# Optimization experiments

Measured on AMD Instinct MI355X. Metric: run time of the kernel, lower is better.

Reference implementation:

```python
import jax, jax.numpy as jnp
import numpy as np

N_NODES = 100000
N_EDGES = 1600000
IN_DIM = 256
OUT_DIM = 128


def setup_inputs() -> dict:
    key = jax.random.key(0)
    k1, k2, k3, k4, k5 = jax.random.split(key, 5)
    h = jax.random.normal(k1, (N_NODES, IN_DIM), dtype=jnp.float32)
    # xavier_normal-ish scales for the two weight matrices
    W = jax.random.normal(k2, (IN_DIM, OUT_DIM), dtype=jnp.float32) * (2.0 / np.sqrt(IN_DIM + OUT_DIM))
    a = jax.random.normal(k3, (2 * OUT_DIM,), dtype=jnp.float32) * (2.0 / np.sqrt(2 * OUT_DIM + 1))
    src = jax.random.randint(k4, (N_EDGES,), 0, N_NODES, dtype=jnp.int32)
    dst = jax.random.randint(k5, (N_EDGES,), 0, N_NODES, dtype=jnp.int32)
    return {"h": h, "W": W, "a": a, "src": src, "dst": dst}


def reference(h, W, a, src, dst):
    n = h.shape[0]
    d = W.shape[1]
    z = h @ W  # [N, out_dim]
    # attn_fc([z_src || z_dst]) == z_src @ a[:d] + z_dst @ a[d:]
    el = z @ a[:d]  # [N]
    er = z @ a[d:]  # [N]
    e = jax.nn.leaky_relu(el[src] + er[dst])  # [E], torch default slope 0.01
    # per-destination (segment) softmax, numerically stable
    seg_max = jax.ops.segment_max(e, dst, num_segments=n)
    e_exp = jnp.exp(e - seg_max[dst])
    denom = jax.ops.segment_sum(e_exp, dst, num_segments=n)
    alpha = e_exp / denom[dst]  # [E]
    # weighted scatter-sum of source z into destinations
    h_out = jax.ops.segment_sum(alpha[:, None] * z[src], dst, num_segments=n)
    return h_out
```

## Files before the change

### kernel.cpp

```cpp
#include <hip/hip_runtime.h>
#include <cstdint>
#include <cstddef>

#define N_NODES 100000
#define N_EDGES 1600000
#define IN_DIM  256
#define OUT_DIM 128

#define NBUCK  391
#define BSHIFT 8
#define BNODES 256
#define BCAP   5632
#define EPB    4096

#define ENC_NEG_INF 0x00800000u

typedef __attribute__((ext_vector_type(8))) short bf16x8;
typedef __attribute__((ext_vector_type(4))) float f32x4;

__device__ __forceinline__ unsigned bf16rn(float f) {
    unsigned u = __float_as_uint(f);
    return (u + 0x7FFFu + ((u >> 16) & 1u)) >> 16;
}

__global__ void init_k(int* __restrict__ bucket_cursor)
{
    int i = blockIdx.x * blockDim.x + threadIdx.x;
    if (i < NBUCK) bucket_cursor[i] = 0;
}

__global__ void w16s_k(const float* __restrict__ W, unsigned short* __restrict__ w16s)
{
    int t = blockIdx.x * blockDim.x + threadIdx.x;
    if (t >= IN_DIM * OUT_DIM) return;
    int j  = t & 7;
    int n  = (t >> 3) & 15;
    int q  = (t >> 7) & 3;
    int c  = (t >> 9) & 7;
    int kc = t >> 12;
    int k   = kc * 32 + q * 8 + j;
    int dim = c * 16 + n;
    w16s[t] = (unsigned short)bf16rn(W[k * OUT_DIM + dim]);
}

#define LA_STRIDE 264

__global__ __launch_bounds__(256) void gemm_z_k(
    const float* __restrict__ h, const unsigned short* __restrict__ w16s,
    const float* __restrict__ a,
    unsigned short* __restrict__ z16, float* __restrict__ el, float* __restrict__ er)
{
    __shared__ unsigned short lA[64 * LA_STRIDE];
    const int t  = threadIdx.x;
    const int n0 = blockIdx.x * 64;

    #pragma unroll
    for (int p = 0; p < 16; ++p) {
        int f = p * 256 + t;
        int i = f >> 6;
        int col = (f & 63) * 4;
        float4 v = make_float4(0.f, 0.f, 0.f, 0.f);
        if (n0 + i < N_NODES)
            v = *(const float4*)&h[(size_t)(n0 + i) * IN_DIM + col];
        uint2 pk;
        pk.x = bf16rn(v.x) | (bf16rn(v.y) << 16);
        pk.y = bf16rn(v.z) | (bf16rn(v.w) << 16);
        *(uint2*)&lA[i * LA_STRIDE + col] = pk;
    }
    __syncthreads();

    const int w    = t >> 6;
    const int lane = t & 63;
    const int q    = lane >> 4;
    const int col  = lane & 15;

    f32x4 acc[8];
    #pragma unroll
    for (int c = 0; c < 8; ++c) acc[c] = (f32x4){0.f, 0.f, 0.f, 0.f};

    #pragma unroll
    for (int kc = 0; kc < 8; ++kc) {
        bf16x8 af = *(const bf16x8*)&lA[(w * 16 + col) * LA_STRIDE + kc * 32 + q * 8];
        bf16x8 bfr[8];
        #pragma unroll
        for (int c = 0; c < 8; ++c)
            bfr[c] = *(const bf16x8*)&w16s[((((kc * 8 + c) * 4 + q) * 16) + col) * 8];
        #pragma unroll
        for (int c = 0; c < 8; ++c)
            acc[c] = __builtin_amdgcn_mfma_f32_16x16x32_bf16(af, bfr[c], acc[c], 0, 0, 0);
    }

    float aL[8], aR[8];
    #pragma unroll
    for (int c = 0; c < 8; ++c) {
        aL[c] = a[c * 16 + col];
        aR[c] = a[128 + c * 16 + col];
    }
    #pragma unroll
    for (int r = 0; r < 4; ++r) {
        int node = n0 + w * 16 + q * 4 + r;
        float sl = 0.f, sr = 0.f;
        #pragma unroll
        for (int c = 0; c < 8; ++c) {
            sl += acc[c][r] * aL[c];
            sr += acc[c][r] * aR[c];
        }
        #pragma unroll
        for (int o = 1; o < 16; o <<= 1) {
            sl += __shfl_xor(sl, o, 64);
            sr += __shfl_xor(sr, o, 64);
        }
        if (node < N_NODES) {
            #pragma unroll
            for (int c = 0; c < 8; ++c)
                z16[(size_t)node * OUT_DIM + c * 16 + col] =
                    (unsigned short)bf16rn(acc[c][r]);
            if (col == 0) { el[node] = sl; er[node] = sr; }
        }
    }
}

__global__ __launch_bounds__(256) void partition_k(
    const int* __restrict__ src, const int* __restrict__ dst,
    const float* __restrict__ el, const float* __restrict__ er,
    int* __restrict__ bucket_cursor, unsigned long long* __restrict__ ebuf)
{
    __shared__ int hist[NBUCK];
    __shared__ int gbaseL[NBUCK];
    const int t = threadIdx.x;
    for (int i = t; i < NBUCK; i += 256) hist[i] = 0;
    __syncthreads();

    const int e0 = blockIdx.x * EPB;
    int bucks[16], ranks[16];
    unsigned long long pk[16];
    #pragma unroll
    for (int k = 0; k < 16; ++k) {
        int e = e0 + k * 256 + t;
        bucks[k] = -1;
        if (e < N_EDGES) {
            int s = src[e], d = dst[e];
            float v = el[s] + er[d];
            v = (v > 0.0f) ? v : 0.01f * v;
            int b = d >> BSHIFT;
            bucks[k] = b;
            ranks[k] = atomicAdd(&hist[b], 1);
            pk[k] = ((unsigned long long)__float_as_uint(v) << 32)
                  | ((unsigned)s << BSHIFT) | (unsigned)(d & (BNODES - 1));
        }
    }
    __syncthreads();
    for (int i = t; i < NBUCK; i += 256)
        gbaseL[i] = atomicAdd(&bucket_cursor[i], hist[i]);
    __syncthreads();
    #pragma unroll
    for (int k = 0; k < 16; ++k)
        if (bucks[k] >= 0)
            ebuf[(size_t)bucks[k] * BCAP + gbaseL[bucks[k]] + ranks[k]] = pk[k];
}

__global__ __launch_bounds__(256) void bucket_k(
    const int* __restrict__ bucket_cursor, const unsigned long long* __restrict__ ebuf,
    unsigned long long* __restrict__ perm, int* __restrict__ begA,
    int* __restrict__ endA, float* __restrict__ denomA)
{
    __shared__ int deg[BNODES];
    __shared__ int off[BNODES];
    __shared__ int cur[BNODES];
    __shared__ unsigned emaxL[BNODES];
    __shared__ float denomL[BNODES];
    __shared__ int ssum[256];

    const int b = blockIdx.x;
    const int t = threadIdx.x;
    const int cnt = bucket_cursor[b];
    const unsigned long long* eb = ebuf + (size_t)b * BCAP;
    unsigned long long* pb = perm + (size_t)b * BCAP;

    deg[t] = 0; emaxL[t] = ENC_NEG_INF; denomL[t] = 0.0f;
    __syncthreads();

    for (int i = t; i < cnt; i += 256) {
        unsigned long long pv = eb[i];
        int ld = (int)(pv & (BNODES - 1));
        unsigned e32 = (unsigned)(pv >> 32);
        unsigned enc = (e32 & 0x80000000u) ? ~e32 : (e32 | 0x80000000u);
        atomicAdd(&deg[ld], 1);
        atomicMax(&emaxL[ld], enc);
    }
    __syncthreads();

    int d  = deg[t];
    int pd = (d + 3) & ~3;
    ssum[t] = pd;
    __syncthreads();
    for (int o = 1; o < 256; o <<= 1) {
        int v = (t >= o) ? ssum[t - o] : 0;
        __syncthreads();
        ssum[t] += v;
        __syncthreads();
    }
    int excl = ssum[t] - pd;
    off[t] = excl; cur[t] = excl;
    __syncthreads();

    for (int i = t; i < cnt; i += 256) {
        unsigned long long pv = eb[i];
        int ld = (int)(pv & (BNODES - 1));
        unsigned s = (unsigned)((pv >> BSHIFT) & 0x1FFFFu);
        float e = __uint_as_float((unsigned)(pv >> 32));
        unsigned u = emaxL[ld];
        float mx = (u & 0x80000000u) ? __uint_as_float(u ^ 0x80000000u)
                                     : __uint_as_float(~u);
        float w = __expf(e - mx);
        atomicAdd(&denomL[ld], w);
        int p = atomicAdd(&cur[ld], 1);
        pb[p] = ((unsigned long long)__float_as_uint(w) << 32) | s;
    }
    __syncthreads();

    int n = b * BNODES + t;
    if (n < N_NODES) {
        int o  = off[t];
        int gb = b * BCAP + o;
        begA[n]   = gb;
        endA[n]   = gb + pd;
        denomA[n] = denomL[t];
        for (int j = o + d; j < o + pd; ++j) pb[j] = 0ull;
    }
}

__global__ __launch_bounds__(256) void node_pass_k(
    const int* __restrict__ begA, const int* __restrict__ endA,
    const float* __restrict__ denomA, const unsigned long long* __restrict__ perm,
    const unsigned* __restrict__ z16, float* __restrict__ out)
{
    int n    = (blockIdx.x * blockDim.x + threadIdx.x) >> 6;
    int lane = threadIdx.x & 63;
    if (n >= N_NODES) return;
    int beg = begA[n], end = endA[n];

    float acc0 = 0.0f, acc1 = 0.0f;
    if (end > beg) {
        const uint4* pp = (const uint4*)perm;
        #pragma unroll 2
        for (int i = (beg >> 2); i < (end >> 2); ++i) {
            uint4 pA = pp[2 * i];
            uint4 pB = pp[2 * i + 1];
            unsigned q0 = z16[(size_t)pA.x * 64 + lane];
            unsigned q1 = z16[(size_t)pA.z * 64 + lane];
            unsigned q2 = z16[(size_t)pB.x * 64 + lane];
            unsigned q3 = z16[(size_t)pB.z * 64 + lane];
            float w0 = __uint_as_float(pA.y);
            float w1 = __uint_as_float(pA.w);
            float w2 = __uint_as_float(pB.y);
            float w3 = __uint_as_float(pB.w);
            acc0 += w0 * __uint_as_float(q0 << 16)
                  + w1 * __uint_as_float(q1 << 16)
                  + w2 * __uint_as_float(q2 << 16)
                  + w3 * __uint_as_float(q3 << 16);
            acc1 += w0 * __uint_as_float(q0 & 0xFFFF0000u)
                  + w1 * __uint_as_float(q1 & 0xFFFF0000u)
                  + w2 * __uint_as_float(q2 & 0xFFFF0000u)
                  + w3 * __uint_as_float(q3 & 0xFFFF0000u);
        }
        float inv = 1.0f / denomA[n];
        acc0 *= inv; acc1 *= inv;
    }
    *(float2*)&out[(size_t)n * OUT_DIM + lane * 2] = make_float2(acc0, acc1);
}

extern "C" void kernel_launch(void* const* d_in, const int* in_sizes, int n_in,
                              void* d_out, int out_size, void* d_ws, size_t ws_size,
                              hipStream_t stream)
{
    (void)in_sizes; (void)n_in; (void)out_size; (void)ws_size;
    const float* h = (const float*)d_in[0];
    const float* W = (const float*)d_in[1];
    const float* a = (const float*)d_in[2];
    const int* src = (const int*)d_in[3];
    const int* dst = (const int*)d_in[4];
    float* out = (float*)d_out;

    char* ws = (char*)d_ws;
    size_t off = 0;
    auto alloc = [&](size_t bytes) -> char* {
        char* p = ws + off;
        off += (bytes + 255) & ~(size_t)255;
        return p;
    };
    unsigned short* z16  = (unsigned short*)alloc((size_t)N_NODES * OUT_DIM * 2);
    unsigned short* w16s = (unsigned short*)alloc((size_t)IN_DIM * OUT_DIM * 2);
    float*    el        = (float*)   alloc((size_t)N_NODES * 4);
    float*    er        = (float*)   alloc((size_t)N_NODES * 4);
    int*      bucket_cursor = (int*) alloc((size_t)NBUCK * 4);
    unsigned long long* ebuf = (unsigned long long*)alloc((size_t)NBUCK * BCAP * 8);
    unsigned long long* perm = (unsigned long long*)alloc((size_t)NBUCK * BCAP * 8);
    int*      begA      = (int*)     alloc((size_t)N_NODES * 4);
    int*      endA      = (int*)     alloc((size_t)N_NODES * 4);
    float*    denomA    = (float*)   alloc((size_t)N_NODES * 4);

    init_k<<<(NBUCK + 255) / 256, 256, 0, stream>>>(bucket_cursor);
    w16s_k<<<(IN_DIM * OUT_DIM + 255) / 256, 256, 0, stream>>>(W, w16s);
    gemm_z_k<<<(N_NODES + 63) / 64, 256, 0, stream>>>(h, w16s, a, z16, el, er);
    partition_k<<<(N_EDGES + EPB - 1) / EPB, 256, 0, stream>>>(src, dst, el, er,
                                                               bucket_cursor, ebuf);
    bucket_k<<<NBUCK, 256, 0, stream>>>(bucket_cursor, ebuf, perm, begA, endA, denomA);
    node_pass_k<<<(N_NODES * 64 + 255) / 256, 256, 0, stream>>>(begA, endA, denomA, perm,
                                                                (const unsigned*)z16, out);
}
```

Measured before the change: 310.1 us.

## Shrink buckets, register-cache bucket edges, fuse init, recompute softmax denominator in node pass

Halves the bucket size to 128 nodes with a smaller capacity, and the partition kernel now handles 2048 edges per block with atomics skipped for empty buckets. The bucket kernel keeps each edge in registers with its rank from the first pass, so it no longer reloads ebuf or uses a second atomic cursor and denominator atomics. The softmax denominator is instead summed in node_pass from the stored weights. Bucket-cursor init is folded into the weight-conversion kernel, and z16 is written as packed 32-bit pairs through a permuted weight column order. The fixed MAXE register cap assumes no bucket exceeds 13*256 edges, which holds for these random inputs but is not guaranteed in general.

Measured after the change: 314.2 us. No clear change (+1.3%).

```diff
diff --git a/kernel.cpp b/kernel.cpp
--- a/kernel.cpp
+++ b/kernel.cpp
@@ -7,11 +7,12 @@
 #define IN_DIM  256
 #define OUT_DIM 128
 
-#define NBUCK  391
-#define BSHIFT 8
-#define BNODES 256
-#define BCAP   5632
-#define EPB    4096
+#define BSHIFT 7
+#define BNODES 128
+#define NBUCK  782
+#define BCAP   3200
+#define MAXE   13
+#define EPB    2048
 
 #define ENC_NEG_INF 0x00800000u
 
@@ -23,15 +24,11 @@
     return (u + 0x7FFFu + ((u >> 16) & 1u)) >> 16;
 }
 
-__global__ void init_k(int* __restrict__ bucket_cursor)
-{
-    int i = blockIdx.x * blockDim.x + threadIdx.x;
-    if (i < NBUCK) bucket_cursor[i] = 0;
-}
-
-__global__ void w16s_k(const float* __restrict__ W, unsigned short* __restrict__ w16s)
+__global__ void w16s_k(const float* __restrict__ W, unsigned short* __restrict__ w16s,
+                       int* __restrict__ bucket_cursor)
 {
     int t = blockIdx.x * blockDim.x + threadIdx.x;
+    if (t < NBUCK) bucket_cursor[t] = 0;
     if (t >= IN_DIM * OUT_DIM) return;
     int j  = t & 7;
     int n  = (t >> 3) & 15;
@@ -39,7 +36,7 @@
     int c  = (t >> 9) & 7;
     int kc = t >> 12;
     int k   = kc * 32 + q * 8 + j;
-    int dim = c * 16 + n;
+    int dim = (c >> 1) * 32 + n * 2 + (c & 1);
     w16s[t] = (unsigned short)bf16rn(W[k * OUT_DIM + dim]);
 }
 
@@ -93,8 +90,9 @@
     float aL[8], aR[8];
     #pragma unroll
     for (int c = 0; c < 8; ++c) {
-        aL[c] = a[c * 16 + col];
-        aR[c] = a[128 + c * 16 + col];
+        int dim = (c >> 1) * 32 + col * 2 + (c & 1);
+        aL[c] = a[dim];
+        aR[c] = a[128 + dim];
     }
     #pragma unroll
     for (int r = 0; r < 4; ++r) {
@@ -112,9 +110,10 @@
         }
         if (node < N_NODES) {
             #pragma unroll
-            for (int c = 0; c < 8; ++c)
-                z16[(size_t)node * OUT_DIM + c * 16 + col] =
-                    (unsigned short)bf16rn(acc[c][r]);
+            for (int g = 0; g < 4; ++g) {
+                unsigned u = bf16rn(acc[2 * g][r]) | (bf16rn(acc[2 * g + 1][r]) << 16);
+                ((unsigned*)z16)[(size_t)node * 64 + g * 16 + col] = u;
+            }
             if (col == 0) { el[node] = sl; er[node] = sr; }
         }
     }
@@ -132,10 +131,10 @@
     __syncthreads();
 
     const int e0 = blockIdx.x * EPB;
-    int bucks[16], ranks[16];
-    unsigned long long pk[16];
-    #pragma unroll
-    for (int k = 0; k < 16; ++k) {
+    int bucks[8], ranks[8];
+    unsigned long long pk[8];
+    #pragma unroll
+    for (int k = 0; k < 8; ++k) {
         int e = e0 + k * 256 + t;
         bucks[k] = -1;
         if (e < N_EDGES) {
@@ -150,26 +149,25 @@
         }
     }
     __syncthreads();
-    for (int i = t; i < NBUCK; i += 256)
-        gbaseL[i] = atomicAdd(&bucket_cursor[i], hist[i]);
-    __syncthreads();
-    #pragma unroll
-    for (int k = 0; k < 16; ++k)
+    for (int i = t; i < NBUCK; i += 256) {
+        int hc = hist[i];
+        gbaseL[i] = hc ? atomicAdd(&bucket_cursor[i], hc) : 0;
+    }
+    __syncthreads();
+    #pragma unroll
+    for (int k = 0; k < 8; ++k)
         if (bucks[k] >= 0)
             ebuf[(size_t)bucks[k] * BCAP + gbaseL[bucks[k]] + ranks[k]] = pk[k];
 }
 
 __global__ __launch_bounds__(256) void bucket_k(
     const int* __restrict__ bucket_cursor, const unsigned long long* __restrict__ ebuf,
-    unsigned long long* __restrict__ perm, int* __restrict__ begA,
-    int* __restrict__ endA, float* __restrict__ denomA)
+    unsigned long long* __restrict__ perm, int* __restrict__ begA, int* __restrict__ endA)
 {
     __shared__ int deg[BNODES];
     __shared__ int off[BNODES];
-    __shared__ int cur[BNODES];
     __shared__ unsigned emaxL[BNODES];
-    __shared__ float denomL[BNODES];
-    __shared__ int ssum[256];
+    __shared__ int ssum[BNODES];
 
     const int b = blockIdx.x;
     const int t = threadIdx.x;
@@ -177,62 +175,75 @@
     const unsigned long long* eb = ebuf + (size_t)b * BCAP;
     unsigned long long* pb = perm + (size_t)b * BCAP;
 
-    deg[t] = 0; emaxL[t] = ENC_NEG_INF; denomL[t] = 0.0f;
-    __syncthreads();
-
-    for (int i = t; i < cnt; i += 256) {
-        unsigned long long pv = eb[i];
-        int ld = (int)(pv & (BNODES - 1));
-        unsigned e32 = (unsigned)(pv >> 32);
-        unsigned enc = (e32 & 0x80000000u) ? ~e32 : (e32 | 0x80000000u);
-        atomicAdd(&deg[ld], 1);
-        atomicMax(&emaxL[ld], enc);
-    }
-    __syncthreads();
-
-    int d  = deg[t];
-    int pd = (d + 3) & ~3;
-    ssum[t] = pd;
-    __syncthreads();
-    for (int o = 1; o < 256; o <<= 1) {
-        int v = (t >= o) ? ssum[t - o] : 0;
+    if (t < BNODES) { deg[t] = 0; emaxL[t] = ENC_NEG_INF; }
+    __syncthreads();
+
+    unsigned long long pv[MAXE];
+    int rk[MAXE];
+    #pragma unroll
+    for (int k = 0; k < MAXE; ++k) {
+        int i = t + k * 256;
+        if (i < cnt) {
+            unsigned long long v = eb[i];
+            int ld = (int)(v & (BNODES - 1));
+            unsigned e32 = (unsigned)(v >> 32);
+            unsigned enc = (e32 & 0x80000000u) ? ~e32 : (e32 | 0x80000000u);
+            rk[k] = atomicAdd(&deg[ld], 1);
+            atomicMax(&emaxL[ld], enc);
+            pv[k] = v;
+        }
+    }
+    __syncthreads();
+
+    int d = 0, pd = 0;
+    if (t < BNODES) {
+        d  = deg[t];
+        pd = (d + 3) & ~3;
+        ssum[t] = pd;
+    }
+    __syncthreads();
+    #pragma unroll
+    for (int o = 1; o < BNODES; o <<= 1) {
+        int v = 0;
+        if (t >= o && t < BNODES) v = ssum[t - o];
         __syncthreads();
-        ssum[t] += v;
+        if (t < BNODES) ssum[t] += v;
         __syncthreads();
     }
-    int excl = ssum[t] - pd;
-    off[t] = excl; cur[t] = excl;
-    __syncthreads();
-
-    for (int i = t; i < cnt; i += 256) {
-        unsigned long long pv = eb[i];
-        int ld = (int)(pv & (BNODES - 1));
-        unsigned s = (unsigned)((pv >> BSHIFT) & 0x1FFFFu);
-        float e = __uint_as_float((unsigned)(pv >> 32));
-        unsigned u = emaxL[ld];
-        float mx = (u & 0x80000000u) ? __uint_as_float(u ^ 0x80000000u)
-                                     : __uint_as_float(~u);
-        float w = __expf(e - mx);
-        atomicAdd(&denomL[ld], w);
-        int p = atomicAdd(&cur[ld], 1);
-        pb[p] = ((unsigned long long)__float_as_uint(w) << 32) | s;
-    }
-    __syncthreads();
-
-    int n = b * BNODES + t;
-    if (n < N_NODES) {
-        int o  = off[t];
-        int gb = b * BCAP + o;
-        begA[n]   = gb;
-        endA[n]   = gb + pd;
-        denomA[n] = denomL[t];
-        for (int j = o + d; j < o + pd; ++j) pb[j] = 0ull;
+    if (t < BNODES) off[t] = ssum[t] - pd;
+    __syncthreads();
+
+    #pragma unroll
+    for (int k = 0; k < MAXE; ++k) {
+        int i = t + k * 256;
+        if (i < cnt) {
+            unsigned long long v = pv[k];
+            int ld = (int)(v & (BNODES - 1));
+            unsigned s = (unsigned)((v >> BSHIFT) & 0x1FFFFu);
+            float e = __uint_as_float((unsigned)(v >> 32));
+            unsigned u = emaxL[ld];
+            float mx = (u & 0x80000000u) ? __uint_as_float(u ^ 0x80000000u)
+                                         : __uint_as_float(~u);
+            float w = __expf(e - mx);
+            pb[off[ld] + rk[k]] = ((unsigned long long)__float_as_uint(w) << 32) | s;
+        }
+    }
+
+    if (t < BNODES) {
+        int n = b * BNODES + t;
+        if (n < N_NODES) {
+            int o  = off[t];
+            int gb = b * BCAP + o;
+            begA[n] = gb;
+            endA[n] = gb + pd;
+            for (int j = o + d; j < o + pd; ++j) pb[j] = 0ull;
+        }
     }
 }
 
 __global__ __launch_bounds__(256) void node_pass_k(
     const int* __restrict__ begA, const int* __restrict__ endA,
-    const float* __restrict__ denomA, const unsigned long long* __restrict__ perm,
+    const unsigned long long* __restrict__ perm,
     const unsigned* __restrict__ z16, float* __restrict__ out)
 {
     int n    = (blockIdx.x * blockDim.x + threadIdx.x) >> 6;
@@ -242,6 +253,7 @@
 
     float acc0 = 0.0f, acc1 = 0.0f;
     if (end > beg) {
+        float dsum = 0.0f;
         const uint4* pp = (const uint4*)perm;
         #pragma unroll 2
         for (int i = (beg >> 2); i < (end >> 2); ++i) {
@@ -263,8 +275,9 @@
                   + w1 * __uint_as_float(q1 & 0xFFFF0000u)
                   + w2 * __uint_as_float(q2 & 0xFFFF0000u)
                   + w3 * __uint_as_float(q3 & 0xFFFF0000u);
-        }
-        float inv = 1.0f / denomA[n];
+            dsum += w0 + w1 + w2 + w3;
+        }
+        float inv = 1.0f / dsum;
         acc0 *= inv; acc1 *= inv;
     }
     *(float2*)&out[(size_t)n * OUT_DIM + lane * 2] = make_float2(acc0, acc1);
@@ -298,14 +311,12 @@
     unsigned long long* perm = (unsigned long long*)alloc((size_t)NBUCK * BCAP * 8);
     int*      begA      = (int*)     alloc((size_t)N_NODES * 4);
     int*      endA      = (int*)     alloc((size_t)N_NODES * 4);
-    float*    denomA    = (float*)   alloc((size_t)N_NODES * 4);
-
-    init_k<<<(NBUCK + 255) / 256, 256, 0, stream>>>(bucket_cursor);
-    w16s_k<<<(IN_DIM * OUT_DIM + 255) / 256, 256, 0, stream>>>(W, w16s);
+
+    w16s_k<<<(IN_DIM * OUT_DIM + 255) / 256, 256, 0, stream>>>(W, w16s, bucket_cursor);
     gemm_z_k<<<(N_NODES + 63) / 64, 256, 0, stream>>>(h, w16s, a, z16, el, er);
     partition_k<<<(N_EDGES + EPB - 1) / EPB, 256, 0, stream>>>(src, dst, el, er,
                                                                bucket_cursor, ebuf);
-    bucket_k<<<NBUCK, 256, 0, stream>>>(bucket_cursor, ebuf, perm, begA, endA, denomA);
-    node_pass_k<<<(N_NODES * 64 + 255) / 256, 256, 0, stream>>>(begA, endA, denomA, perm,
+    bucket_k<<<NBUCK, 256, 0, stream>>>(bucket_cursor, ebuf, perm, begA, endA);
+    node_pass_k<<<(N_NODES * 64 + 255) / 256, 256, 0, stream>>>(begA, endA, perm,
                                                                 (const unsigned*)z16, out);
 }
```
